# Kernel optimization log

Hardware: AMD Instinct MI355X
Metric: run time of the kernel (lower is better)

Reference implementation:

```python
import jax, jax.numpy as jnp
import numpy as np

D_VISION = 1024
D_BRANCH = 256
N_BRANCHES = 4
N_HEADS = 4
HEAD_DIM = D_BRANCH // N_HEADS
DIVERSITY_WEIGHT = 0.1
LN_EPS = 1e-5


def setup_inputs() -> dict:
    key = jax.random.key(0)
    ks = jax.random.split(key, 8)
    B, T, N = 8, 16, 256
    frame_patches = jax.random.normal(ks[0], (B, T, N, D_VISION), dtype=jnp.float32)
    # LayerNorm params (shared input_norm)
    ln_gamma = jnp.ones((D_VISION,), jnp.float32)
    ln_beta = jnp.zeros((D_VISION,), jnp.float32)
    # Per-branch params stacked on a leading branch dim
    query = jax.random.normal(ks[1], (N_BRANCHES, N_HEADS, HEAD_DIM), jnp.float32) * 0.02
    wstd = 1.0 / np.sqrt(D_VISION)
    Wk = jax.random.uniform(ks[2], (N_BRANCHES, D_VISION, D_BRANCH), jnp.float32, -wstd, wstd)
    bk = jax.random.uniform(ks[3], (N_BRANCHES, D_BRANCH), jnp.float32, -wstd, wstd)
    Wv = jax.random.uniform(ks[4], (N_BRANCHES, D_VISION, D_BRANCH), jnp.float32, -wstd, wstd)
    bv = jax.random.uniform(ks[5], (N_BRANCHES, D_BRANCH), jnp.float32, -wstd, wstd)
    ostd = 1.0 / np.sqrt(D_BRANCH)
    Wo = jax.random.uniform(ks[6], (N_BRANCHES, D_BRANCH, D_BRANCH), jnp.float32, -ostd, ostd)
    bo = jax.random.uniform(ks[7], (N_BRANCHES, D_BRANCH), jnp.float32, -ostd, ostd)
    return dict(frame_patches=frame_patches, ln_gamma=ln_gamma, ln_beta=ln_beta,
                query=query, Wk=Wk, bk=bk, Wv=Wv, bv=bv, Wo=Wo, bo=bo)


def _layernorm(x, g, b):
    mu = jnp.mean(x, axis=-1, keepdims=True)
    var = jnp.var(x, axis=-1, keepdims=True)
    return (x - mu) * jax.lax.rsqrt(var + LN_EPS) * g + b


def reference(frame_patches, ln_gamma, ln_beta, query, Wk, bk, Wv, bv, Wo, bo):
    B, T, N, D = frame_patches.shape
    nb, H, hd = query.shape
    db = H * hd
    scale = hd ** -0.5
    x = _layernorm(frame_patches.reshape(B * T, N, D), ln_gamma, ln_beta)  # (BT, N, D)
    # Batched k/v projections across all branches (the fusion opportunity)
    k = (jnp.einsum('bpd,ndk->nbpk', x, Wk) + bk[:, None, None, :]).reshape(nb, B * T, N, H, hd)
    v = (jnp.einsum('bpd,ndk->nbpk', x, Wv) + bv[:, None, None, :]).reshape(nb, B * T, N, H, hd)
    # Single learnable query per (branch, head) attends over patches
    scores = jnp.einsum('nbphd,nhd->nbhp', k, query) * scale  # (nb, BT, H, N)
    attn = jax.nn.softmax(scores, axis=-1)
    attn_avg = attn.mean(axis=2)  # (nb, BT, N) head-averaged, pre-dropout
    # Dropout is inference no-op (eval mode)
    pooled = jnp.einsum('nbhp,nbphd->nbhd', attn, v).reshape(nb, B * T, db)
    out = jnp.einsum('nbk,nkj->nbj', pooled, Wo) + bo[:, None, :]  # (nb, BT, db)
    streams = out.transpose(1, 0, 2).reshape(B, T, nb, db)
    # Diversity loss: mean pairwise cosine similarity of attention distributions
    norms = jnp.maximum(jnp.linalg.norm(attn_avg, axis=-1, keepdims=True), 1e-8)
    a = attn_avg / norms
    sims = jnp.einsum('ibn,jbn->ijb', a, a).mean(axis=-1)  # (nb, nb)
    mask = jnp.triu(jnp.ones((nb, nb), attn_avg.dtype), k=1)
    diversity_loss = DIVERSITY_WEIGHT * (sims * mask).sum() / mask.sum()
    return streams, diversity_loss
```

## Files before the change

### kernel.cpp

```cpp
#include <hip/hip_runtime.h>
#include <stdint.h>

#define BT      128
#define NPATCH  256
#define DV      1024
#define NB      4
#define DB      256
#define NH16    16
#define SCALE   0.125f
#define LNEPS   1e-5f

#define OFF_BWS    16384u
#define OFF_PSC    24608u
#define OFF_DRAW   25120u
#define OFF_STATS  549408u
#define OFF_W      614944u
#define OFF_CV     1139232u
#define OFF_DIV    1141280u
#define OFF_XBAR   1142048u
#define OFF_POOL   9530656u
#define XSLICE     2097152u

#define LROW 264

typedef short bf16x8 __attribute__((ext_vector_type(8)));
typedef float f32x4  __attribute__((ext_vector_type(4)));

__device__ __forceinline__ short f2bf(float f) {
    union { float f; unsigned u; } v; v.f = f;
    unsigned u = v.u;
    unsigned r = (u + 0x7fffu + ((u >> 16) & 1u)) >> 16;
    return (short)r;
}

__device__ __forceinline__ unsigned pk2(float lo, float hi) {
    union { float f; unsigned u; } a, b; a.f = lo; b.f = hi;
    return __builtin_amdgcn_perm(b.u, a.u, 0x07060302u);
}

__global__ __launch_bounds__(256) void kP(const float* __restrict__ Wk,
                                          const float* __restrict__ q,
                                          const float* __restrict__ g,
                                          const float* __restrict__ b,
                                          float* __restrict__ ws) {
    const int nh = blockIdx.x >> 4, ich = blockIdx.x & 15;
    const int n = nh >> 2, h = nh & 3;
    __shared__ float qs[64];
    __shared__ float redS[4], redC[4];
    const int t = threadIdx.x;
    if (t < 64) qs[t] = q[nh * 64 + t];
    __syncthreads();
    const int r = t >> 2, qd = t & 3;
    const int i = ich * 64 + r;
    const float* wrow = Wk + ((size_t)n * DV + i) * DB + h * 64 + qd * 16;
    float acc = 0.f;
    #pragma unroll
    for (int d = 0; d < 16; d += 4) {
        float4 w4 = *(const float4*)(wrow + d);
        acc += w4.x * qs[qd * 16 + d]     + w4.y * qs[qd * 16 + d + 1]
             + w4.z * qs[qd * 16 + d + 2] + w4.w * qs[qd * 16 + d + 3];
    }
    acc += __shfl_xor(acc, 1);
    acc += __shfl_xor(acc, 2);
    float gw = g[i] * acc;
    if (qd == 0) {
        unsigned short* bws = (unsigned short*)(ws + OFF_BWS);
        const int kt = i >> 5, oct = (r >> 3) & 3, j = r & 7;
        bws[((kt * 64 + oct * 16 + nh) << 3) + j] = (unsigned short)f2bf(gw);
    }
    float mS = (qd == 0) ? gw : 0.f;
    float mC = (qd == 0) ? b[i] * acc : 0.f;
    #pragma unroll
    for (int dd = 4; dd < 64; dd <<= 1) { mS += __shfl_xor(mS, dd); mC += __shfl_xor(mC, dd); }
    const int wave = t >> 6, lane = t & 63;
    if (lane == 0) { redS[wave] = mS; redC[wave] = mC; }
    __syncthreads();
    if (t == 0) {
        ws[OFF_PSC + (nh * 16 + ich) * 2 + 0] = redS[0] + redS[1] + redS[2] + redS[3];
        ws[OFF_PSC + (nh * 16 + ich) * 2 + 1] = redC[0] + redC[1] + redC[2] + redC[3];
    }
}

__global__ __launch_bounds__(256) void kA(const float* __restrict__ x,
                                          float* __restrict__ ws) {
    __shared__ unsigned short xs[64 * LROW];
    const int t = threadIdx.x;
    const int wv = t >> 6, lane = t & 63;
    const int m = lane & 15, oct = lane >> 4;
    const int row0 = blockIdx.x * 64;
    const bf16x8* bfp = (const bf16x8*)((const unsigned short*)(ws + OFF_BWS));
    const float* xb = x + (size_t)row0 * DV;

    float sum[16], sq[16];
    #pragma unroll
    for (int i = 0; i < 16; ++i) { sum[i] = 0.f; sq[i] = 0.f; }
    f32x4 acc = {0.f, 0.f, 0.f, 0.f};
    float4 r[16];

    auto loadr = [&](int c) {
        #pragma unroll
        for (int i = 0; i < 16; ++i)
            r[i] = *(const float4*)(xb + (size_t)(i * 4 + wv) * DV + c * 256 + lane * 4);
    };
    auto commit = [&]() {
        #pragma unroll
        for (int i = 0; i < 16; ++i) {
            float4 v = r[i];
            sum[i] += v.x + v.y + v.z + v.w;
            sq[i]  += v.x * v.x + v.y * v.y + v.z * v.z + v.w * v.w;
            uint2 pk; pk.x = pk2(v.x, v.y); pk.y = pk2(v.z, v.w);
            *(uint2*)&xs[(i * 4 + wv) * LROW + lane * 4] = pk;
        }
    };
    auto comp = [&](int c) {
        #pragma unroll
        for (int kt = 0; kt < 8; ++kt) {
            bf16x8 af = *(const bf16x8*)&xs[(wv * 16 + m) * LROW + kt * 32 + oct * 8];
            bf16x8 bf = bfp[(c * 8 + kt) * 64 + lane];
            acc = __builtin_amdgcn_mfma_f32_16x16x32_bf16(af, bf, acc, 0, 0, 0);
        }
    };

    loadr(0);
    for (int c = 0; c < 4; ++c) {
        __syncthreads();
        commit();
        __syncthreads();
        if (c < 3) loadr(c + 1);
        comp(c);
    }

    #pragma unroll
    for (int r2 = 0; r2 < 4; ++r2)
        ws[OFF_DRAW + (size_t)(row0 + wv * 16 + oct * 4 + r2) * 16 + m] = acc[r2];

    #pragma unroll
    for (int i = 0; i < 16; ++i) {
        float s = sum[i], q2 = sq[i];
        #pragma unroll
        for (int d = 1; d < 64; d <<= 1) { s += __shfl_xor(s, d); q2 += __shfl_xor(q2, d); }
        if (lane == 0) {
            const int row = row0 + i * 4 + wv;
            const float mu  = s * (1.f / 1024.f);
            const float var = q2 * (1.f / 1024.f) - mu * mu;
            float2 st; st.x = mu; st.y = rsqrtf(var + LNEPS);
            *(float2*)(ws + OFF_STATS + (size_t)row * 2) = st;
        }
    }
}

__global__ __launch_bounds__(256) void kC(const float* __restrict__ x,
                                          const float* __restrict__ q,
                                          const float* __restrict__ bk,
                                          float* __restrict__ ws) {
    const int bt = blockIdx.x;
    const int qq = blockIdx.y;
    const int t = threadIdx.x;
    __shared__ __attribute__((aligned(16))) float s_s[NH16 * NPATCH];
    __shared__ __attribute__((aligned(16))) float aavg[NB * NPATCH];
    __shared__ __attribute__((aligned(16))) float w_s[64 * 16];
    __shared__ __attribute__((aligned(16))) float rstd_s[NPATCH];
    __shared__ __attribute__((aligned(16))) float mrs[NPATCH];
    __shared__ float Ss[NH16], Cbs[NH16];

    {
        const int nh = t >> 4, ich = t & 15;
        float S = ws[OFF_PSC + t * 2 + 0];
        float C = ws[OFF_PSC + t * 2 + 1];
        const int n2 = nh >> 2, h2 = nh & 3;
        const float* bkp = bk + n2 * DB + h2 * 64 + ich * 4;
        const float* qp  = q + nh * 64 + ich * 4;
        C += bkp[0] * qp[0] + bkp[1] * qp[1] + bkp[2] * qp[2] + bkp[3] * qp[3];
        #pragma unroll
        for (int d = 1; d < 16; d <<= 1) { S += __shfl_xor(S, d); C += __shfl_xor(C, d); }
        if (ich == 0) { Ss[nh] = S; Cbs[nh] = C; }
    }
    const size_t row = (size_t)bt * NPATCH + t;
    const float2 st = *(const float2*)(ws + OFF_STATS + row * 2);
    rstd_s[t] = st.y;
    mrs[t] = st.x * st.y;
    __syncthreads();

    const float* dr = ws + OFF_DRAW + row * 16;
    #pragma unroll
    for (int nh = 0; nh < NH16; ++nh)
        s_s[nh * NPATCH + t] = (st.y * (dr[nh] - st.x * Ss[nh]) + Cbs[nh]) * SCALE;
    __syncthreads();

    const int wave = t >> 6, lane = t & 63;
    for (int r = 0; r < 4; ++r) {
        const int nh = wave * 4 + r;
        float4 v = *(float4*)&s_s[nh * NPATCH + lane * 4];
        float mx = fmaxf(fmaxf(v.x, v.y), fmaxf(v.z, v.w));
        for (int d = 1; d < 64; d <<= 1) mx = fmaxf(mx, __shfl_xor(mx, d));
        float e0 = __expf(v.x - mx), e1 = __expf(v.y - mx);
        float e2 = __expf(v.z - mx), e3 = __expf(v.w - mx);
        float s = e0 + e1 + e2 + e3;
        for (int d = 1; d < 64; d <<= 1) s += __shfl_xor(s, d);
        float inv = 1.f / s;
        float4 a; a.x = e0 * inv; a.y = e1 * inv; a.z = e2 * inv; a.w = e3 * inv;
        *(float4*)&s_s[nh * NPATCH + lane * 4] = a;
    }
    __syncthreads();

    if (qq == 0) {
        for (int r = 0; r < 4; ++r) {
            const int nh = wave * 4 + r;
            float4 a4 = *(float4*)&s_s[nh * NPATCH + lane * 4];
            float4 m4 = *(float4*)&mrs[lane * 4];
            float dd = a4.x * m4.x + a4.y * m4.y + a4.z * m4.z + a4.w * m4.w;
            for (int d = 1; d < 64; d <<= 1) dd += __shfl_xor(dd, d);
            if (lane == 0) ws[OFF_CV + bt * NH16 + nh] = dd;
        }
        #pragma unroll
        for (int nb2 = 0; nb2 < NB; ++nb2)
            aavg[nb2 * NPATCH + t] = 0.25f * (s_s[(nb2 * 4 + 0) * NPATCH + t] + s_s[(nb2 * 4 + 1) * NPATCH + t]
                                            + s_s[(nb2 * 4 + 2) * NPATCH + t] + s_s[(nb2 * 4 + 3) * NPATCH + t]);
        __syncthreads();
        if (wave == 0) {
            float nrm[NB];
            #pragma unroll
            for (int nb2 = 0; nb2 < NB; ++nb2) {
                float4 v = *(float4*)&aavg[nb2 * NPATCH + lane * 4];
                float ss = v.x * v.x + v.y * v.y + v.z * v.z + v.w * v.w;
                for (int d = 1; d < 64; d <<= 1) ss += __shfl_xor(ss, d);
                nrm[nb2] = fmaxf(sqrtf(ss), 1e-8f);
            }
            int pi = 0;
            for (int i2 = 0; i2 < NB; ++i2)
                for (int j2 = i2 + 1; j2 < NB; ++j2) {
                    float4 va = *(float4*)&aavg[i2 * NPATCH + lane * 4];
                    float4 vb = *(float4*)&aavg[j2 * NPATCH + lane * 4];
                    float dd = va.x * vb.x + va.y * vb.y + va.z * vb.z + va.w * vb.w;
                    for (int d = 1; d < 64; d <<= 1) dd += __shfl_xor(dd, d);
                    if (lane == 0) ws[OFF_DIV + bt * 6 + pi] = dd / (nrm[i2] * nrm[j2]);
                    ++pi;
                }
        }
    }

    for (int idx = t; idx < 1024; idx += 256) {
        const int p = idx >> 4, nh = idx & 15;
        w_s[idx] = s_s[nh * NPATCH + qq * 64 + p] * rstd_s[qq * 64 + p];
    }
    __syncthreads();

    float4 acc[16];
    #pragma unroll
    for (int i = 0; i < 16; ++i) { acc[i].x = 0.f; acc[i].y = 0.f; acc[i].z = 0.f; acc[i].w = 0.f; }
    const float* xp = x + (size_t)(bt * NPATCH + qq * 64) * DV + t * 4;
    #define FMA4(k, wgt, xv) acc[k].x += (wgt) * xv.x; acc[k].y += (wgt) * xv.y; \
                             acc[k].z += (wgt) * xv.z; acc[k].w += (wgt) * xv.w;
    #define PBLOCK(p, xv) { \
        float4 a0 = *(const float4*)&w_s[(p) * 16 + 0]; \
        float4 a1 = *(const float4*)&w_s[(p) * 16 + 4]; \
        float4 a2 = *(const float4*)&w_s[(p) * 16 + 8]; \
        float4 a3 = *(const float4*)&w_s[(p) * 16 + 12]; \
        FMA4(0, a0.x, xv)  FMA4(1, a0.y, xv)  FMA4(2, a0.z, xv)  FMA4(3, a0.w, xv) \
        FMA4(4, a1.x, xv)  FMA4(5, a1.y, xv)  FMA4(6, a1.z, xv)  FMA4(7, a1.w, xv) \
        FMA4(8, a2.x, xv)  FMA4(9, a2.y, xv)  FMA4(10, a2.z, xv) FMA4(11, a2.w, xv) \
        FMA4(12, a3.x, xv) FMA4(13, a3.y, xv) FMA4(14, a3.z, xv) FMA4(15, a3.w, xv) }
    for (int p = 0; p < 16; ++p) {
        float4 xv0 = *(const float4*)(xp + (size_t)(p +  0) * DV);
        float4 xv1 = *(const float4*)(xp + (size_t)(p + 16) * DV);
        float4 xv2 = *(const float4*)(xp + (size_t)(p + 32) * DV);
        float4 xv3 = *(const float4*)(xp + (size_t)(p + 48) * DV);
        PBLOCK(p, xv0)
        PBLOCK(p + 16, xv1)
        PBLOCK(p + 32, xv2)
        PBLOCK(p + 48, xv3)
    }
    #undef PBLOCK
    #undef FMA4
    #pragma unroll
    for (int nh = 0; nh < 16; ++nh)
        *(float4*)(ws + OFF_XBAR + (size_t)qq * XSLICE
                   + ((size_t)bt * NH16 + nh) * DV + t * 4) = acc[nh];
}

__global__ __launch_bounds__(256) void kD1(const float* __restrict__ Wv,
                                           const float* __restrict__ g,
                                           const float* __restrict__ b,
                                           const float* __restrict__ bv,
                                           float* __restrict__ ws) {
    const int nh = blockIdx.x & 15, btg = blockIdx.x >> 4;
    const int n = nh >> 2, h = nh & 3;
    const int bt0 = btg * 4, cb = h * 64;
    __shared__ __attribute__((aligned(16))) float xs[4][1024];
    __shared__ __attribute__((aligned(16))) float gs[1024], bs[1024];
    __shared__ float red[4][64][6];
    const int t = threadIdx.x;
    for (int e = t; e < 1024; e += 256) {
        const int bt = e >> 8, i4 = e & 255;
        const size_t b0 = OFF_XBAR + ((size_t)(bt0 + bt) * NH16 + nh) * DV + i4 * 4;
        float4 s = {0.f, 0.f, 0.f, 0.f};
        #pragma unroll
        for (int qq = 0; qq < 4; ++qq) {
            float4 v = *(const float4*)(ws + b0 + (size_t)qq * XSLICE);
            s.x += v.x; s.y += v.y; s.z += v.z; s.w += v.w;
        }
        *(float4*)&xs[bt][i4 * 4] = s;
    }
    for (int e = t; e < 1024; e += 256) { gs[e] = g[e]; bs[e] = b[e]; }
    __syncthreads();
    const int c = t & 63, sub = t >> 6;
    float acc[4];
    #pragma unroll
    for (int l = 0; l < 4; ++l) acc[l] = 0.f;
    float gv = 0.f, bvv = 0.f;
    const float* wvp = Wv + ((size_t)n * DV + sub * 256) * DB + cb + c;
    const int ib0 = sub * 256;
    #pragma unroll 2
    for (int gidx = 0; gidx < 64; ++gidx) {
        const int ib = ib0 + gidx * 4;
        float w0 = wvp[(size_t)(gidx * 4 + 0) * DB];
        float w1 = wvp[(size_t)(gidx * 4 + 1) * DB];
        float w2 = wvp[(size_t)(gidx * 4 + 2) * DB];
        float w3 = wvp[(size_t)(gidx * 4 + 3) * DB];
        float4 g4 = *(const float4*)&gs[ib];
        float4 b4 = *(const float4*)&bs[ib];
        float q0 = g4.x * w0, q1 = g4.y * w1, q2 = g4.z * w2, q3 = g4.w * w3;
        gv  += q0 + q1 + q2 + q3;
        bvv += b4.x * w0 + b4.y * w1 + b4.z * w2 + b4.w * w3;
        #pragma unroll
        for (int l = 0; l < 4; ++l) {
            float4 xr = *(const float4*)&xs[l][ib];
            acc[l] += xr.x * q0 + xr.y * q1 + xr.z * q2 + xr.w * q3;
        }
    }
    #pragma unroll
    for (int l = 0; l < 4; ++l) red[sub][c][l] = acc[l];
    red[sub][c][4] = gv; red[sub][c][5] = bvv;
    __syncthreads();
    const int c2 = t & 63, l = t >> 6;
    float gvS = red[0][c2][4] + red[1][c2][4] + red[2][c2][4] + red[3][c2][4];
    float bvS = red[0][c2][5] + red[1][c2][5] + red[2][c2][5] + red[3][c2][5];
    float base = bv[n * DB + cb + c2] + bvS;
    float p = red[0][c2][l] + red[1][c2][l] + red[2][c2][l] + red[3][c2][l];
    float C = ws[OFF_CV + (bt0 + l) * NH16 + nh];
    ws[OFF_POOL + ((size_t)n * BT + bt0 + l) * DB + cb + c2] = p - C * gvS + base;
}

__global__ __launch_bounds__(256) void kD2(const float* __restrict__ Wo,
                                           const float* __restrict__ bo,
                                           const float* __restrict__ ws,
                                           float* __restrict__ out) {
    const int btg = blockIdx.x & 15, jq = (blockIdx.x >> 4) & 3, n = blockIdx.x >> 6;
    const int bt0 = btg * 8, j0 = jq * 64;
    __shared__ __attribute__((aligned(16))) float ps[8][256];
    __shared__ float red[4][64][8];
    __shared__ float dred[4];
    const int t = threadIdx.x;
    for (int e = t; e < 512; e += 256) {
        const int bt = e >> 6, c4 = e & 63;
        *(float4*)&ps[bt][c4 * 4] =
            *(const float4*)(ws + OFF_POOL + ((size_t)n * BT + bt0 + bt) * DB + c4 * 4);
    }
    float dacc = 0.f;
    if (blockIdx.x == 0)
        for (int idx = t; idx < 768; idx += 256) dacc += ws[OFF_DIV + idx];
    for (int d = 1; d < 64; d <<= 1) dacc += __shfl_xor(dacc, d);
    if ((t & 63) == 0) dred[t >> 6] = dacc;
    __syncthreads();
    if (blockIdx.x == 0 && t == 0)
        out[131072] = 0.1f * (dred[0] + dred[1] + dred[2] + dred[3]) / 768.f;
    const int j = t & 63, sub = t >> 6;
    float acc[8];
    #pragma unroll
    for (int l = 0; l < 8; ++l) acc[l] = 0.f;
    const float* wop = Wo + ((size_t)n * DB + sub * 64) * DB + j0 + j;
    const int cb0 = sub * 64;
    #pragma unroll 2
    for (int gidx = 0; gidx < 16; ++gidx) {
        const int cb = cb0 + gidx * 4;
        float w0 = wop[(size_t)(gidx * 4 + 0) * DB];
        float w1 = wop[(size_t)(gidx * 4 + 1) * DB];
        float w2 = wop[(size_t)(gidx * 4 + 2) * DB];
        float w3 = wop[(size_t)(gidx * 4 + 3) * DB];
        #pragma unroll
        for (int l = 0; l < 8; ++l) {
            float4 pr = *(const float4*)&ps[l][cb];
            acc[l] += pr.x * w0 + pr.y * w1 + pr.z * w2 + pr.w * w3;
        }
    }
    #pragma unroll
    for (int l = 0; l < 8; ++l) red[sub][j][l] = acc[l];
    __syncthreads();
    const int j2 = t & 63, l0 = t >> 6;
    float bov = bo[n * DB + j0 + j2];
    #pragma unroll
    for (int li = 0; li < 2; ++li) {
        const int l = l0 + li * 4;
        float o = red[0][j2][l] + red[1][j2][l] + red[2][j2][l] + red[3][j2][l] + bov;
        out[((size_t)(bt0 + l) * NB + n) * DB + j0 + j2] = o;
    }
}

extern "C" void kernel_launch(void* const* d_in, const int* in_sizes, int n_in,
                              void* d_out, int out_size, void* d_ws, size_t ws_size,
                              hipStream_t stream) {
    const float* x  = (const float*)d_in[0];
    const float* g  = (const float*)d_in[1];
    const float* b  = (const float*)d_in[2];
    const float* q  = (const float*)d_in[3];
    const float* Wk = (const float*)d_in[4];
    const float* bk = (const float*)d_in[5];
    const float* Wv = (const float*)d_in[6];
    const float* bv = (const float*)d_in[7];
    const float* Wo = (const float*)d_in[8];
    const float* bo = (const float*)d_in[9];
    float* out = (float*)d_out;
    float* ws  = (float*)d_ws;

    hipLaunchKernelGGL(kP,  dim3(256),    dim3(256), 0, stream, Wk, q, g, b, ws);
    hipLaunchKernelGGL(kA,  dim3(512),    dim3(256), 0, stream, x, ws);
    hipLaunchKernelGGL(kC,  dim3(128, 4), dim3(256), 0, stream, x, q, bk, ws);
    hipLaunchKernelGGL(kD1, dim3(512),    dim3(256), 0, stream, Wv, g, b, bv, ws);
    hipLaunchKernelGGL(kD2, dim3(256),    dim3(256), 0, stream, Wo, bo, ws, out);
}
```

Baseline: 281.0 us.

## Fuse five kernels into one persistent kernel with grid-wide barriers

Merges the five separate launches (Wk·q projection, x·B MFMA with LN stats, softmax/xbar accumulation, Wv pooling, Wo output) into a single 512-block kernel that separates phases with atomic-counter grid barriers. A memset resets the barrier counters before each launch. The intent is to remove launch gaps and tail effects between the stages. The risk is that the spin barriers deadlock or serialize if all 512 blocks are not co-resident; launch_bounds(256,2) and the spin cap only mitigate this.

Result: slower. 554.6 us (+97.4%).

```diff
diff --git a/kernel.cpp b/kernel.cpp
--- a/kernel.cpp
+++ b/kernel.cpp
@@ -9,12 +9,12 @@
 #define NH16    16
 #define SCALE   0.125f
 #define LNEPS   1e-5f
+#define NBLK    512
 
 #define OFF_BWS    16384u
 #define OFF_PSC    24608u
 #define OFF_DRAW   25120u
 #define OFF_STATS  549408u
-#define OFF_W      614944u
 #define OFF_CV     1139232u
 #define OFF_DIV    1141280u
 #define OFF_XBAR   1142048u
@@ -38,361 +38,384 @@
     return __builtin_amdgcn_perm(b.u, a.u, 0x07060302u);
 }
 
-__global__ __launch_bounds__(256) void kP(const float* __restrict__ Wk,
-                                          const float* __restrict__ q,
-                                          const float* __restrict__ g,
-                                          const float* __restrict__ b,
-                                          float* __restrict__ ws) {
-    const int nh = blockIdx.x >> 4, ich = blockIdx.x & 15;
-    const int n = nh >> 2, h = nh & 3;
-    __shared__ float qs[64];
-    __shared__ float redS[4], redC[4];
-    const int t = threadIdx.x;
-    if (t < 64) qs[t] = q[nh * 64 + t];
+__device__ __forceinline__ void gridbar(int* bar, int phase) {
     __syncthreads();
-    const int r = t >> 2, qd = t & 3;
-    const int i = ich * 64 + r;
-    const float* wrow = Wk + ((size_t)n * DV + i) * DB + h * 64 + qd * 16;
-    float acc = 0.f;
-    #pragma unroll
-    for (int d = 0; d < 16; d += 4) {
-        float4 w4 = *(const float4*)(wrow + d);
-        acc += w4.x * qs[qd * 16 + d]     + w4.y * qs[qd * 16 + d + 1]
-             + w4.z * qs[qd * 16 + d + 2] + w4.w * qs[qd * 16 + d + 3];
-    }
-    acc += __shfl_xor(acc, 1);
-    acc += __shfl_xor(acc, 2);
-    float gw = g[i] * acc;
-    if (qd == 0) {
-        unsigned short* bws = (unsigned short*)(ws + OFF_BWS);
-        const int kt = i >> 5, oct = (r >> 3) & 3, j = r & 7;
-        bws[((kt * 64 + oct * 16 + nh) << 3) + j] = (unsigned short)f2bf(gw);
-    }
-    float mS = (qd == 0) ? gw : 0.f;
-    float mC = (qd == 0) ? b[i] * acc : 0.f;
-    #pragma unroll
-    for (int dd = 4; dd < 64; dd <<= 1) { mS += __shfl_xor(mS, dd); mC += __shfl_xor(mC, dd); }
-    const int wave = t >> 6, lane = t & 63;
-    if (lane == 0) { redS[wave] = mS; redC[wave] = mC; }
+    if (threadIdx.x == 0) {
+        __threadfence();
+        __hip_atomic_fetch_add(&bar[phase], 1, __ATOMIC_ACQ_REL,
+                               __HIP_MEMORY_SCOPE_AGENT);
+        int spins = 0;
+        while (__hip_atomic_load(&bar[phase], __ATOMIC_ACQUIRE,
+                                 __HIP_MEMORY_SCOPE_AGENT) < NBLK
+               && spins < (1 << 21)) {
+            ++spins;
+            __builtin_amdgcn_s_sleep(8);
+        }
+        __threadfence();
+    }
     __syncthreads();
-    if (t == 0) {
-        ws[OFF_PSC + (nh * 16 + ich) * 2 + 0] = redS[0] + redS[1] + redS[2] + redS[3];
-        ws[OFF_PSC + (nh * 16 + ich) * 2 + 1] = redC[0] + redC[1] + redC[2] + redC[3];
-    }
 }
 
-__global__ __launch_bounds__(256) void kA(const float* __restrict__ x,
-                                          float* __restrict__ ws) {
-    __shared__ unsigned short xs[64 * LROW];
-    const int t = threadIdx.x;
-    const int wv = t >> 6, lane = t & 63;
-    const int m = lane & 15, oct = lane >> 4;
-    const int row0 = blockIdx.x * 64;
-    const bf16x8* bfp = (const bf16x8*)((const unsigned short*)(ws + OFF_BWS));
-    const float* xb = x + (size_t)row0 * DV;
-
-    float sum[16], sq[16];
-    #pragma unroll
-    for (int i = 0; i < 16; ++i) { sum[i] = 0.f; sq[i] = 0.f; }
-    f32x4 acc = {0.f, 0.f, 0.f, 0.f};
-    float4 r[16];
-
-    auto loadr = [&](int c) {
-        #pragma unroll
-        for (int i = 0; i < 16; ++i)
-            r[i] = *(const float4*)(xb + (size_t)(i * 4 + wv) * DV + c * 256 + lane * 4);
-    };
-    auto commit = [&]() {
+__global__ __launch_bounds__(256, 2) void kMega(
+    const float* __restrict__ x,  const float* __restrict__ g,
+    const float* __restrict__ b,  const float* __restrict__ q,
+    const float* __restrict__ Wk, const float* __restrict__ bk,
+    const float* __restrict__ Wv, const float* __restrict__ bv,
+    const float* __restrict__ Wo, const float* __restrict__ bo,
+    float* __restrict__ ws, float* __restrict__ out)
+{
+    __shared__ __attribute__((aligned(16))) float smf[8448];
+    int* bar = (int*)ws;
+    const int t   = threadIdx.x;
+    const int blk = blockIdx.x;
+
+    if (blk < 256) {
+        float* qs   = smf;
+        float* redS = smf + 64;
+        float* redC = smf + 68;
+        const int nh = blk >> 4, ich = blk & 15;
+        const int n = nh >> 2, h = nh & 3;
+        if (t < 64) qs[t] = q[nh * 64 + t];
+        __syncthreads();
+        const int r = t >> 2, qd = t & 3;
+        const int i = ich * 64 + r;
+        const float* wrow = Wk + ((size_t)n * DV + i) * DB + h * 64 + qd * 16;
+        float acc = 0.f;
+        #pragma unroll
+        for (int d = 0; d < 16; d += 4) {
+            float4 w4 = *(const float4*)(wrow + d);
+            acc += w4.x * qs[qd * 16 + d]     + w4.y * qs[qd * 16 + d + 1]
+                 + w4.z * qs[qd * 16 + d + 2] + w4.w * qs[qd * 16 + d + 3];
+        }
+        acc += __shfl_xor(acc, 1);
+        acc += __shfl_xor(acc, 2);
+        float gw = g[i] * acc;
+        if (qd == 0) {
+            unsigned short* bws = (unsigned short*)(ws + OFF_BWS);
+            const int kt = i >> 5, oct = (r >> 3) & 3, j = r & 7;
+            bws[((kt * 64 + oct * 16 + nh) << 3) + j] = (unsigned short)f2bf(gw);
+        }
+        float mS = (qd == 0) ? gw : 0.f;
+        float mC = (qd == 0) ? b[i] * acc : 0.f;
+        #pragma unroll
+        for (int dd = 4; dd < 64; dd <<= 1) { mS += __shfl_xor(mS, dd); mC += __shfl_xor(mC, dd); }
+        const int wave = t >> 6, lane = t & 63;
+        if (lane == 0) { redS[wave] = mS; redC[wave] = mC; }
+        __syncthreads();
+        if (t == 0) {
+            ws[OFF_PSC + (nh * 16 + ich) * 2 + 0] = redS[0] + redS[1] + redS[2] + redS[3];
+            ws[OFF_PSC + (nh * 16 + ich) * 2 + 1] = redC[0] + redC[1] + redC[2] + redC[3];
+        }
+    }
+    gridbar(bar, 0);
+
+    {
+        unsigned short* xs = (unsigned short*)smf;
+        const int wv = t >> 6, lane = t & 63;
+        const int m = lane & 15, oct = lane >> 4;
+        const int row0 = blk * 64;
+        const bf16x8* bfp = (const bf16x8*)((const unsigned short*)(ws + OFF_BWS));
+        const float* xb = x + (size_t)row0 * DV;
+
+        float sum[16], sq[16];
+        #pragma unroll
+        for (int i = 0; i < 16; ++i) { sum[i] = 0.f; sq[i] = 0.f; }
+        f32x4 acc = {0.f, 0.f, 0.f, 0.f};
+        float4 r[16];
+
+        auto loadr = [&](int c) {
+            #pragma unroll
+            for (int i = 0; i < 16; ++i)
+                r[i] = *(const float4*)(xb + (size_t)(i * 4 + wv) * DV + c * 256 + lane * 4);
+        };
+        auto commit = [&]() {
+            #pragma unroll
+            for (int i = 0; i < 16; ++i) {
+                float4 v = r[i];
+                sum[i] += v.x + v.y + v.z + v.w;
+                sq[i]  += v.x * v.x + v.y * v.y + v.z * v.z + v.w * v.w;
+                uint2 pk; pk.x = pk2(v.x, v.y); pk.y = pk2(v.z, v.w);
+                *(uint2*)&xs[(i * 4 + wv) * LROW + lane * 4] = pk;
+            }
+        };
+        auto comp = [&](int c) {
+            #pragma unroll
+            for (int kt = 0; kt < 8; ++kt) {
+                bf16x8 af = *(const bf16x8*)&xs[(wv * 16 + m) * LROW + kt * 32 + oct * 8];
+                bf16x8 bf = bfp[(c * 8 + kt) * 64 + lane];
+                acc = __builtin_amdgcn_mfma_f32_16x16x32_bf16(af, bf, acc, 0, 0, 0);
+            }
+        };
+
+        loadr(0);
+        for (int c = 0; c < 4; ++c) {
+            __syncthreads();
+            commit();
+            __syncthreads();
+            if (c < 3) loadr(c + 1);
+            comp(c);
+        }
+
+        #pragma unroll
+        for (int r2 = 0; r2 < 4; ++r2)
+            ws[OFF_DRAW + (size_t)(row0 + wv * 16 + oct * 4 + r2) * 16 + m] = acc[r2];
+
         #pragma unroll
         for (int i = 0; i < 16; ++i) {
-            float4 v = r[i];
-            sum[i] += v.x + v.y + v.z + v.w;
-            sq[i]  += v.x * v.x + v.y * v.y + v.z * v.z + v.w * v.w;
-            uint2 pk; pk.x = pk2(v.x, v.y); pk.y = pk2(v.z, v.w);
-            *(uint2*)&xs[(i * 4 + wv) * LROW + lane * 4] = pk;
-        }
-    };
-    auto comp = [&](int c) {
-        #pragma unroll
-        for (int kt = 0; kt < 8; ++kt) {
-            bf16x8 af = *(const bf16x8*)&xs[(wv * 16 + m) * LROW + kt * 32 + oct * 8];
-            bf16x8 bf = bfp[(c * 8 + kt) * 64 + lane];
-            acc = __builtin_amdgcn_mfma_f32_16x16x32_bf16(af, bf, acc, 0, 0, 0);
-        }
-    };
-
-    loadr(0);
-    for (int c = 0; c < 4; ++c) {
-        __syncthreads();
-        commit();
-        __syncthreads();
-        if (c < 3) loadr(c + 1);
-        comp(c);
-    }
-
-    #pragma unroll
-    for (int r2 = 0; r2 < 4; ++r2)
-        ws[OFF_DRAW + (size_t)(row0 + wv * 16 + oct * 4 + r2) * 16 + m] = acc[r2];
-
-    #pragma unroll
-    for (int i = 0; i < 16; ++i) {
-        float s = sum[i], q2 = sq[i];
-        #pragma unroll
-        for (int d = 1; d < 64; d <<= 1) { s += __shfl_xor(s, d); q2 += __shfl_xor(q2, d); }
-        if (lane == 0) {
-            const int row = row0 + i * 4 + wv;
-            const float mu  = s * (1.f / 1024.f);
-            const float var = q2 * (1.f / 1024.f) - mu * mu;
-            float2 st; st.x = mu; st.y = rsqrtf(var + LNEPS);
-            *(float2*)(ws + OFF_STATS + (size_t)row * 2) = st;
-        }
-    }
-}
-
-__global__ __launch_bounds__(256) void kC(const float* __restrict__ x,
-                                          const float* __restrict__ q,
-                                          const float* __restrict__ bk,
-                                          float* __restrict__ ws) {
-    const int bt = blockIdx.x;
-    const int qq = blockIdx.y;
-    const int t = threadIdx.x;
-    __shared__ __attribute__((aligned(16))) float s_s[NH16 * NPATCH];
-    __shared__ __attribute__((aligned(16))) float aavg[NB * NPATCH];
-    __shared__ __attribute__((aligned(16))) float w_s[64 * 16];
-    __shared__ __attribute__((aligned(16))) float rstd_s[NPATCH];
-    __shared__ __attribute__((aligned(16))) float mrs[NPATCH];
-    __shared__ float Ss[NH16], Cbs[NH16];
+            float s = sum[i], q2 = sq[i];
+            #pragma unroll
+            for (int d = 1; d < 64; d <<= 1) { s += __shfl_xor(s, d); q2 += __shfl_xor(q2, d); }
+            if (lane == 0) {
+                const int row = row0 + i * 4 + wv;
+                const float mu  = s * (1.f / 1024.f);
+                const float var = q2 * (1.f / 1024.f) - mu * mu;
+                float2 st; st.x = mu; st.y = rsqrtf(var + LNEPS);
+                *(float2*)(ws + OFF_STATS + (size_t)row * 2) = st;
+            }
+        }
+    }
+    gridbar(bar, 1);
 
     {
-        const int nh = t >> 4, ich = t & 15;
-        float S = ws[OFF_PSC + t * 2 + 0];
-        float C = ws[OFF_PSC + t * 2 + 1];
-        const int n2 = nh >> 2, h2 = nh & 3;
-        const float* bkp = bk + n2 * DB + h2 * 64 + ich * 4;
-        const float* qp  = q + nh * 64 + ich * 4;
-        C += bkp[0] * qp[0] + bkp[1] * qp[1] + bkp[2] * qp[2] + bkp[3] * qp[3];
-        #pragma unroll
-        for (int d = 1; d < 16; d <<= 1) { S += __shfl_xor(S, d); C += __shfl_xor(C, d); }
-        if (ich == 0) { Ss[nh] = S; Cbs[nh] = C; }
-    }
-    const size_t row = (size_t)bt * NPATCH + t;
-    const float2 st = *(const float2*)(ws + OFF_STATS + row * 2);
-    rstd_s[t] = st.y;
-    mrs[t] = st.x * st.y;
-    __syncthreads();
-
-    const float* dr = ws + OFF_DRAW + row * 16;
-    #pragma unroll
-    for (int nh = 0; nh < NH16; ++nh)
-        s_s[nh * NPATCH + t] = (st.y * (dr[nh] - st.x * Ss[nh]) + Cbs[nh]) * SCALE;
-    __syncthreads();
-
-    const int wave = t >> 6, lane = t & 63;
-    for (int r = 0; r < 4; ++r) {
-        const int nh = wave * 4 + r;
-        float4 v = *(float4*)&s_s[nh * NPATCH + lane * 4];
-        float mx = fmaxf(fmaxf(v.x, v.y), fmaxf(v.z, v.w));
-        for (int d = 1; d < 64; d <<= 1) mx = fmaxf(mx, __shfl_xor(mx, d));
-        float e0 = __expf(v.x - mx), e1 = __expf(v.y - mx);
-        float e2 = __expf(v.z - mx), e3 = __expf(v.w - mx);
-        float s = e0 + e1 + e2 + e3;
-        for (int d = 1; d < 64; d <<= 1) s += __shfl_xor(s, d);
-        float inv = 1.f / s;
-        float4 a; a.x = e0 * inv; a.y = e1 * inv; a.z = e2 * inv; a.w = e3 * inv;
-        *(float4*)&s_s[nh * NPATCH + lane * 4] = a;
-    }
-    __syncthreads();
-
-    if (qq == 0) {
+        const int bt = blk & 127;
+        const int qq = blk >> 7;
+        float* s_s    = smf;
+        float* aavg   = smf + 4096;
+        float* w_s    = smf + 5120;
+        float* rstd_s = smf + 6144;
+        float* mrs    = smf + 6400;
+        float* Ss     = smf + 6656;
+        float* Cbs    = smf + 6672;
+
+        {
+            const int nh = t >> 4, ich = t & 15;
+            float S = ws[OFF_PSC + t * 2 + 0];
+            float C = ws[OFF_PSC + t * 2 + 1];
+            const int n2 = nh >> 2, h2 = nh & 3;
+            const float* bkp = bk + n2 * DB + h2 * 64 + ich * 4;
+            const float* qp  = q + nh * 64 + ich * 4;
+            C += bkp[0] * qp[0] + bkp[1] * qp[1] + bkp[2] * qp[2] + bkp[3] * qp[3];
+            #pragma unroll
+            for (int d = 1; d < 16; d <<= 1) { S += __shfl_xor(S, d); C += __shfl_xor(C, d); }
+            if (ich == 0) { Ss[nh] = S; Cbs[nh] = C; }
+        }
+        const size_t row = (size_t)bt * NPATCH + t;
+        const float2 st = *(const float2*)(ws + OFF_STATS + row * 2);
+        rstd_s[t] = st.y;
+        mrs[t] = st.x * st.y;
+        __syncthreads();
+
+        const float* dr = ws + OFF_DRAW + row * 16;
+        #pragma unroll
+        for (int nh = 0; nh < NH16; ++nh)
+            s_s[nh * NPATCH + t] = (st.y * (dr[nh] - st.x * Ss[nh]) + Cbs[nh]) * SCALE;
+        __syncthreads();
+
+        const int wave = t >> 6, lane = t & 63;
         for (int r = 0; r < 4; ++r) {
             const int nh = wave * 4 + r;
-            float4 a4 = *(float4*)&s_s[nh * NPATCH + lane * 4];
-            float4 m4 = *(float4*)&mrs[lane * 4];
-            float dd = a4.x * m4.x + a4.y * m4.y + a4.z * m4.z + a4.w * m4.w;
-            for (int d = 1; d < 64; d <<= 1) dd += __shfl_xor(dd, d);
-            if (lane == 0) ws[OFF_CV + bt * NH16 + nh] = dd;
-        }
-        #pragma unroll
-        for (int nb2 = 0; nb2 < NB; ++nb2)
-            aavg[nb2 * NPATCH + t] = 0.25f * (s_s[(nb2 * 4 + 0) * NPATCH + t] + s_s[(nb2 * 4 + 1) * NPATCH + t]
-                                            + s_s[(nb2 * 4 + 2) * NPATCH + t] + s_s[(nb2 * 4 + 3) * NPATCH + t]);
-        __syncthreads();
-        if (wave == 0) {
-            float nrm[NB];
-            #pragma unroll
-            for (int nb2 = 0; nb2 < NB; ++nb2) {
-                float4 v = *(float4*)&aavg[nb2 * NPATCH + lane * 4];
-                float ss = v.x * v.x + v.y * v.y + v.z * v.z + v.w * v.w;
-                for (int d = 1; d < 64; d <<= 1) ss += __shfl_xor(ss, d);
-                nrm[nb2] = fmaxf(sqrtf(ss), 1e-8f);
-            }
-            int pi = 0;
-            for (int i2 = 0; i2 < NB; ++i2)
-                for (int j2 = i2 + 1; j2 < NB; ++j2) {
-                    float4 va = *(float4*)&aavg[i2 * NPATCH + lane * 4];
-                    float4 vb = *(float4*)&aavg[j2 * NPATCH + lane * 4];
-                    float dd = va.x * vb.x + va.y * vb.y + va.z * vb.z + va.w * vb.w;
-                    for (int d = 1; d < 64; d <<= 1) dd += __shfl_xor(dd, d);
-                    if (lane == 0) ws[OFF_DIV + bt * 6 + pi] = dd / (nrm[i2] * nrm[j2]);
-                    ++pi;
+            float4 v = *(float4*)&s_s[nh * NPATCH + lane * 4];
+            float mx = fmaxf(fmaxf(v.x, v.y), fmaxf(v.z, v.w));
+            for (int d = 1; d < 64; d <<= 1) mx = fmaxf(mx, __shfl_xor(mx, d));
+            float e0 = __expf(v.x - mx), e1 = __expf(v.y - mx);
+            float e2 = __expf(v.z - mx), e3 = __expf(v.w - mx);
+            float s = e0 + e1 + e2 + e3;
+            for (int d = 1; d < 64; d <<= 1) s += __shfl_xor(s, d);
+            float inv = 1.f / s;
+            float4 a; a.x = e0 * inv; a.y = e1 * inv; a.z = e2 * inv; a.w = e3 * inv;
+            *(float4*)&s_s[nh * NPATCH + lane * 4] = a;
+        }
+        __syncthreads();
+
+        if (qq == 0) {
+            for (int r = 0; r < 4; ++r) {
+                const int nh = wave * 4 + r;
+                float4 a4 = *(float4*)&s_s[nh * NPATCH + lane * 4];
+                float4 m4 = *(float4*)&mrs[lane * 4];
+                float dd = a4.x * m4.x + a4.y * m4.y + a4.z * m4.z + a4.w * m4.w;
+                for (int d = 1; d < 64; d <<= 1) dd += __shfl_xor(dd, d);
+                if (lane == 0) ws[OFF_CV + bt * NH16 + nh] = dd;
+            }
+            #pragma unroll
+            for (int nb2 = 0; nb2 < NB; ++nb2)
+                aavg[nb2 * NPATCH + t] = 0.25f * (s_s[(nb2 * 4 + 0) * NPATCH + t] + s_s[(nb2 * 4 + 1) * NPATCH + t]
+                                                + s_s[(nb2 * 4 + 2) * NPATCH + t] + s_s[(nb2 * 4 + 3) * NPATCH + t]);
+            __syncthreads();
+            if (wave == 0) {
+                float nrm[NB];
+                #pragma unroll
+                for (int nb2 = 0; nb2 < NB; ++nb2) {
+                    float4 v = *(float4*)&aavg[nb2 * NPATCH + lane * 4];
+                    float ss = v.x * v.x + v.y * v.y + v.z * v.z + v.w * v.w;
+                    for (int d = 1; d < 64; d <<= 1) ss += __shfl_xor(ss, d);
+                    nrm[nb2] = fmaxf(sqrtf(ss), 1e-8f);
                 }
-        }
-    }
-
-    for (int idx = t; idx < 1024; idx += 256) {
-        const int p = idx >> 4, nh = idx & 15;
-        w_s[idx] = s_s[nh * NPATCH + qq * 64 + p] * rstd_s[qq * 64 + p];
-    }
-    __syncthreads();
-
-    float4 acc[16];
-    #pragma unroll
-    for (int i = 0; i < 16; ++i) { acc[i].x = 0.f; acc[i].y = 0.f; acc[i].z = 0.f; acc[i].w = 0.f; }
-    const float* xp = x + (size_t)(bt * NPATCH + qq * 64) * DV + t * 4;
-    #define FMA4(k, wgt, xv) acc[k].x += (wgt) * xv.x; acc[k].y += (wgt) * xv.y; \
-                             acc[k].z += (wgt) * xv.z; acc[k].w += (wgt) * xv.w;
-    #define PBLOCK(p, xv) { \
-        float4 a0 = *(const float4*)&w_s[(p) * 16 + 0]; \
-        float4 a1 = *(const float4*)&w_s[(p) * 16 + 4]; \
-        float4 a2 = *(const float4*)&w_s[(p) * 16 + 8]; \
-        float4 a3 = *(const float4*)&w_s[(p) * 16 + 12]; \
-        FMA4(0, a0.x, xv)  FMA4(1, a0.y, xv)  FMA4(2, a0.z, xv)  FMA4(3, a0.w, xv) \
-        FMA4(4, a1.x, xv)  FMA4(5, a1.y, xv)  FMA4(6, a1.z, xv)  FMA4(7, a1.w, xv) \
-        FMA4(8, a2.x, xv)  FMA4(9, a2.y, xv)  FMA4(10, a2.z, xv) FMA4(11, a2.w, xv) \
-        FMA4(12, a3.x, xv) FMA4(13, a3.y, xv) FMA4(14, a3.z, xv) FMA4(15, a3.w, xv) }
-    for (int p = 0; p < 16; ++p) {
-        float4 xv0 = *(const float4*)(xp + (size_t)(p +  0) * DV);
-        float4 xv1 = *(const float4*)(xp + (size_t)(p + 16) * DV);
-        float4 xv2 = *(const float4*)(xp + (size_t)(p + 32) * DV);
-        float4 xv3 = *(const float4*)(xp + (size_t)(p + 48) * DV);
-        PBLOCK(p, xv0)
-        PBLOCK(p + 16, xv1)
-        PBLOCK(p + 32, xv2)
-        PBLOCK(p + 48, xv3)
-    }
-    #undef PBLOCK
-    #undef FMA4
-    #pragma unroll
-    for (int nh = 0; nh < 16; ++nh)
-        *(float4*)(ws + OFF_XBAR + (size_t)qq * XSLICE
-                   + ((size_t)bt * NH16 + nh) * DV + t * 4) = acc[nh];
-}
-
-__global__ __launch_bounds__(256) void kD1(const float* __restrict__ Wv,
-                                           const float* __restrict__ g,
-                                           const float* __restrict__ b,
-                                           const float* __restrict__ bv,
-                                           float* __restrict__ ws) {
-    const int nh = blockIdx.x & 15, btg = blockIdx.x >> 4;
-    const int n = nh >> 2, h = nh & 3;
-    const int bt0 = btg * 4, cb = h * 64;
-    __shared__ __attribute__((aligned(16))) float xs[4][1024];
-    __shared__ __attribute__((aligned(16))) float gs[1024], bs[1024];
-    __shared__ float red[4][64][6];
-    const int t = threadIdx.x;
-    for (int e = t; e < 1024; e += 256) {
-        const int bt = e >> 8, i4 = e & 255;
-        const size_t b0 = OFF_XBAR + ((size_t)(bt0 + bt) * NH16 + nh) * DV + i4 * 4;
-        float4 s = {0.f, 0.f, 0.f, 0.f};
-        #pragma unroll
-        for (int qq = 0; qq < 4; ++qq) {
-            float4 v = *(const float4*)(ws + b0 + (size_t)qq * XSLICE);
-            s.x += v.x; s.y += v.y; s.z += v.z; s.w += v.w;
-        }
-        *(float4*)&xs[bt][i4 * 4] = s;
-    }
-    for (int e = t; e < 1024; e += 256) { gs[e] = g[e]; bs[e] = b[e]; }
-    __syncthreads();
-    const int c = t & 63, sub = t >> 6;
-    float acc[4];
-    #pragma unroll
-    for (int l = 0; l < 4; ++l) acc[l] = 0.f;
-    float gv = 0.f, bvv = 0.f;
-    const float* wvp = Wv + ((size_t)n * DV + sub * 256) * DB + cb + c;
-    const int ib0 = sub * 256;
-    #pragma unroll 2
-    for (int gidx = 0; gidx < 64; ++gidx) {
-        const int ib = ib0 + gidx * 4;
-        float w0 = wvp[(size_t)(gidx * 4 + 0) * DB];
-        float w1 = wvp[(size_t)(gidx * 4 + 1) * DB];
-        float w2 = wvp[(size_t)(gidx * 4 + 2) * DB];
-        float w3 = wvp[(size_t)(gidx * 4 + 3) * DB];
-        float4 g4 = *(const float4*)&gs[ib];
-        float4 b4 = *(const float4*)&bs[ib];
-        float q0 = g4.x * w0, q1 = g4.y * w1, q2 = g4.z * w2, q3 = g4.w * w3;
-        gv  += q0 + q1 + q2 + q3;
-        bvv += b4.x * w0 + b4.y * w1 + b4.z * w2 + b4.w * w3;
-        #pragma unroll
-        for (int l = 0; l < 4; ++l) {
-            float4 xr = *(const float4*)&xs[l][ib];
-            acc[l] += xr.x * q0 + xr.y * q1 + xr.z * q2 + xr.w * q3;
-        }
-    }
-    #pragma unroll
-    for (int l = 0; l < 4; ++l) red[sub][c][l] = acc[l];
-    red[sub][c][4] = gv; red[sub][c][5] = bvv;
-    __syncthreads();
-    const int c2 = t & 63, l = t >> 6;
-    float gvS = red[0][c2][4] + red[1][c2][4] + red[2][c2][4] + red[3][c2][4];
-    float bvS = red[0][c2][5] + red[1][c2][5] + red[2][c2][5] + red[3][c2][5];
-    float base = bv[n * DB + cb + c2] + bvS;
-    float p = red[0][c2][l] + red[1][c2][l] + red[2][c2][l] + red[3][c2][l];
-    float C = ws[OFF_CV + (bt0 + l) * NH16 + nh];
-    ws[OFF_POOL + ((size_t)n * BT + bt0 + l) * DB + cb + c2] = p - C * gvS + base;
-}
-
-__global__ __launch_bounds__(256) void kD2(const float* __restrict__ Wo,
-                                           const float* __restrict__ bo,
-                                           const float* __restrict__ ws,
-                                           float* __restrict__ out) {
-    const int btg = blockIdx.x & 15, jq = (blockIdx.x >> 4) & 3, n = blockIdx.x >> 6;
-    const int bt0 = btg * 8, j0 = jq * 64;
-    __shared__ __attribute__((aligned(16))) float ps[8][256];
-    __shared__ float red[4][64][8];
-    __shared__ float dred[4];
-    const int t = threadIdx.x;
-    for (int e = t; e < 512; e += 256) {
-        const int bt = e >> 6, c4 = e & 63;
-        *(float4*)&ps[bt][c4 * 4] =
-            *(const float4*)(ws + OFF_POOL + ((size_t)n * BT + bt0 + bt) * DB + c4 * 4);
-    }
-    float dacc = 0.f;
-    if (blockIdx.x == 0)
-        for (int idx = t; idx < 768; idx += 256) dacc += ws[OFF_DIV + idx];
-    for (int d = 1; d < 64; d <<= 1) dacc += __shfl_xor(dacc, d);
-    if ((t & 63) == 0) dred[t >> 6] = dacc;
-    __syncthreads();
-    if (blockIdx.x == 0 && t == 0)
-        out[131072] = 0.1f * (dred[0] + dred[1] + dred[2] + dred[3]) / 768.f;
-    const int j = t & 63, sub = t >> 6;
-    float acc[8];
-    #pragma unroll
-    for (int l = 0; l < 8; ++l) acc[l] = 0.f;
-    const float* wop = Wo + ((size_t)n * DB + sub * 64) * DB + j0 + j;
-    const int cb0 = sub * 64;
-    #pragma unroll 2
-    for (int gidx = 0; gidx < 16; ++gidx) {
-        const int cb = cb0 + gidx * 4;
-        float w0 = wop[(size_t)(gidx * 4 + 0) * DB];
-        float w1 = wop[(size_t)(gidx * 4 + 1) * DB];
-        float w2 = wop[(size_t)(gidx * 4 + 2) * DB];
-        float w3 = wop[(size_t)(gidx * 4 + 3) * DB];
-        #pragma unroll
-        for (int l = 0; l < 8; ++l) {
-            float4 pr = *(const float4*)&ps[l][cb];
-            acc[l] += pr.x * w0 + pr.y * w1 + pr.z * w2 + pr.w * w3;
-        }
-    }
-    #pragma unroll
-    for (int l = 0; l < 8; ++l) red[sub][j][l] = acc[l];
-    __syncthreads();
-    const int j2 = t & 63, l0 = t >> 6;
-    float bov = bo[n * DB + j0 + j2];
-    #pragma unroll
-    for (int li = 0; li < 2; ++li) {
-        const int l = l0 + li * 4;
-        float o = red[0][j2][l] + red[1][j2][l] + red[2][j2][l] + red[3][j2][l] + bov;
-        out[((size_t)(bt0 + l) * NB + n) * DB + j0 + j2] = o;
+                int pi = 0;
+                for (int i2 = 0; i2 < NB; ++i2)
+                    for (int j2 = i2 + 1; j2 < NB; ++j2) {
+                        float4 va = *(float4*)&aavg[i2 * NPATCH + lane * 4];
+                        float4 vb = *(float4*)&aavg[j2 * NPATCH + lane * 4];
+                        float dd = va.x * vb.x + va.y * vb.y + va.z * vb.z + va.w * vb.w;
+                        for (int d = 1; d < 64; d <<= 1) dd += __shfl_xor(dd, d);
+                        if (lane == 0) ws[OFF_DIV + bt * 6 + pi] = dd / (nrm[i2] * nrm[j2]);
+                        ++pi;
+                    }
+            }
+        }
+
+        for (int idx = t; idx < 1024; idx += 256) {
+            const int p = idx >> 4, nh = idx & 15;
+            w_s[idx] = s_s[nh * NPATCH + qq * 64 + p] * rstd_s[qq * 64 + p];
+        }
+        __syncthreads();
+
+        float4 acc[16];
+        #pragma unroll
+        for (int i = 0; i < 16; ++i) { acc[i].x = 0.f; acc[i].y = 0.f; acc[i].z = 0.f; acc[i].w = 0.f; }
+        const float* xp = x + (size_t)(bt * NPATCH + qq * 64) * DV + t * 4;
+        #define FMA4(k, wgt, xv) acc[k].x += (wgt) * xv.x; acc[k].y += (wgt) * xv.y; \
+                                 acc[k].z += (wgt) * xv.z; acc[k].w += (wgt) * xv.w;
+        #define PBLOCK(p, xv) { \
+            float4 a0 = *(const float4*)&w_s[(p) * 16 + 0]; \
+            float4 a1 = *(const float4*)&w_s[(p) * 16 + 4]; \
+            float4 a2 = *(const float4*)&w_s[(p) * 16 + 8]; \
+            float4 a3 = *(const float4*)&w_s[(p) * 16 + 12]; \
+            FMA4(0, a0.x, xv)  FMA4(1, a0.y, xv)  FMA4(2, a0.z, xv)  FMA4(3, a0.w, xv) \
+            FMA4(4, a1.x, xv)  FMA4(5, a1.y, xv)  FMA4(6, a1.z, xv)  FMA4(7, a1.w, xv) \
+            FMA4(8, a2.x, xv)  FMA4(9, a2.y, xv)  FMA4(10, a2.z, xv) FMA4(11, a2.w, xv) \
+            FMA4(12, a3.x, xv) FMA4(13, a3.y, xv) FMA4(14, a3.z, xv) FMA4(15, a3.w, xv) }
+        for (int p = 0; p < 16; ++p) {
+            float4 xv0 = *(const float4*)(xp + (size_t)(p +  0) * DV);
+            float4 xv1 = *(const float4*)(xp + (size_t)(p + 16) * DV);
+            float4 xv2 = *(const float4*)(xp + (size_t)(p + 32) * DV);
+            float4 xv3 = *(const float4*)(xp + (size_t)(p + 48) * DV);
+            PBLOCK(p, xv0)
+            PBLOCK(p + 16, xv1)
+            PBLOCK(p + 32, xv2)
+            PBLOCK(p + 48, xv3)
+        }
+        #undef PBLOCK
+        #undef FMA4
+        #pragma unroll
+        for (int nh = 0; nh < 16; ++nh)
+            *(float4*)(ws + OFF_XBAR + (size_t)qq * XSLICE
+                       + ((size_t)bt * NH16 + nh) * DV + t * 4) = acc[nh];
+    }
+    gridbar(bar, 2);
+
+    {
+        const int nh = blk & 15, btg = blk >> 4;
+        const int n = nh >> 2, h = nh & 3;
+        const int bt0 = btg * 4, cb = h * 64;
+        float* xs4 = smf;
+        float* gs  = smf + 4096;
+        float* bs  = smf + 5120;
+        float* red = smf + 6144;
+        #define RED1(s_, c_, l_) red[(((s_) * 64) + (c_)) * 6 + (l_)]
+        for (int e = t; e < 1024; e += 256) {
+            const int bt = e >> 8, i4 = e & 255;
+            const size_t b0 = OFF_XBAR + ((size_t)(bt0 + bt) * NH16 + nh) * DV + i4 * 4;
+            float4 s = {0.f, 0.f, 0.f, 0.f};
+            #pragma unroll
+            for (int qq = 0; qq < 4; ++qq) {
+                float4 v = *(const float4*)(ws + b0 + (size_t)qq * XSLICE);
+                s.x += v.x; s.y += v.y; s.z += v.z; s.w += v.w;
+            }
+            *(float4*)&xs4[bt * 1024 + i4 * 4] = s;
+        }
+        for (int e = t; e < 1024; e += 256) { gs[e] = g[e]; bs[e] = b[e]; }
+        __syncthreads();
+        const int c = t & 63, sub = t >> 6;
+        float acc[4];
+        #pragma unroll
+        for (int l = 0; l < 4; ++l) acc[l] = 0.f;
+        float gv = 0.f, bvv = 0.f;
+        const float* wvp = Wv + ((size_t)n * DV + sub * 256) * DB + cb + c;
+        const int ib0 = sub * 256;
+        #pragma unroll 2
+        for (int gidx = 0; gidx < 64; ++gidx) {
+            const int ib = ib0 + gidx * 4;
+            float w0 = wvp[(size_t)(gidx * 4 + 0) * DB];
+            float w1 = wvp[(size_t)(gidx * 4 + 1) * DB];
+            float w2 = wvp[(size_t)(gidx * 4 + 2) * DB];
+            float w3 = wvp[(size_t)(gidx * 4 + 3) * DB];
+            float4 g4 = *(const float4*)&gs[ib];
+            float4 b4 = *(const float4*)&bs[ib];
+            float q0 = g4.x * w0, q1 = g4.y * w1, q2 = g4.z * w2, q3 = g4.w * w3;
+            gv  += q0 + q1 + q2 + q3;
+            bvv += b4.x * w0 + b4.y * w1 + b4.z * w2 + b4.w * w3;
+            #pragma unroll
+            for (int l = 0; l < 4; ++l) {
+                const float* xr = &xs4[l * 1024 + ib];
+                acc[l] += xr[0] * q0 + xr[1] * q1 + xr[2] * q2 + xr[3] * q3;
+            }
+        }
+        #pragma unroll
+        for (int l = 0; l < 4; ++l) RED1(sub, c, l) = acc[l];
+        RED1(sub, c, 4) = gv; RED1(sub, c, 5) = bvv;
+        __syncthreads();
+        const int c2 = t & 63, l = t >> 6;
+        float gvS = RED1(0, c2, 4) + RED1(1, c2, 4) + RED1(2, c2, 4) + RED1(3, c2, 4);
+        float bvS = RED1(0, c2, 5) + RED1(1, c2, 5) + RED1(2, c2, 5) + RED1(3, c2, 5);
+        float base = bv[n * DB + cb + c2] + bvS;
+        float p = RED1(0, c2, l) + RED1(1, c2, l) + RED1(2, c2, l) + RED1(3, c2, l);
+        float C = ws[OFF_CV + (bt0 + l) * NH16 + nh];
+        ws[OFF_POOL + ((size_t)n * BT + bt0 + l) * DB + cb + c2] = p - C * gvS + base;
+        #undef RED1
+    }
+    gridbar(bar, 3);
+
+    if (blk < 256) {
+        const int btg = blk & 15, jq = (blk >> 4) & 3, n = blk >> 6;
+        const int bt0 = btg * 8, j0 = jq * 64;
+        float* ps   = smf;
+        float* red  = smf + 2048;
+        float* dred = smf + 4096;
+        #define RED2(s_, j_, l_) red[(((s_) * 64) + (j_)) * 8 + (l_)]
+        for (int e = t; e < 512; e += 256) {
+            const int bt = e >> 6, c4 = e & 63;
+            *(float4*)&ps[bt * 256 + c4 * 4] =
+                *(const float4*)(ws + OFF_POOL + ((size_t)n * BT + bt0 + bt) * DB + c4 * 4);
+        }
+        float dacc = 0.f;
+        if (blk == 0)
+            for (int idx = t; idx < 768; idx += 256) dacc += ws[OFF_DIV + idx];
+        for (int d = 1; d < 64; d <<= 1) dacc += __shfl_xor(dacc, d);
+        if ((t & 63) == 0) dred[t >> 6] = dacc;
+        __syncthreads();
+        if (blk == 0 && t == 0)
+            out[131072] = 0.1f * (dred[0] + dred[1] + dred[2] + dred[3]) / 768.f;
+        const int j = t & 63, sub = t >> 6;
+        float acc[8];
+        #pragma unroll
+        for (int l = 0; l < 8; ++l) acc[l] = 0.f;
+        const float* wop = Wo + ((size_t)n * DB + sub * 64) * DB + j0 + j;
+        const int cb0 = sub * 64;
+        #pragma unroll 2
+        for (int gidx = 0; gidx < 16; ++gidx) {
+            const int cb = cb0 + gidx * 4;
+            float w0 = wop[(size_t)(gidx * 4 + 0) * DB];
+            float w1 = wop[(size_t)(gidx * 4 + 1) * DB];
+            float w2 = wop[(size_t)(gidx * 4 + 2) * DB];
+            float w3 = wop[(size_t)(gidx * 4 + 3) * DB];
+            #pragma unroll
+            for (int l = 0; l < 8; ++l) {
+                const float* pr = &ps[l * 256 + cb];
+                acc[l] += pr[0] * w0 + pr[1] * w1 + pr[2] * w2 + pr[3] * w3;
+            }
+        }
+        #pragma unroll
+        for (int l = 0; l < 8; ++l) RED2(sub, j, l) = acc[l];
+        __syncthreads();
+        const int j2 = t & 63, l0 = t >> 6;
+        float bov = bo[n * DB + j0 + j2];
+        #pragma unroll
+        for (int li = 0; li < 2; ++li) {
+            const int l = l0 + li * 4;
+            float o = RED2(0, j2, l) + RED2(1, j2, l) + RED2(2, j2, l) + RED2(3, j2, l) + bov;
+            out[((size_t)(bt0 + l) * NB + n) * DB + j0 + j2] = o;
+        }
+        #undef RED2
     }
 }
 
@@ -412,9 +435,7 @@
     float* out = (float*)d_out;
     float* ws  = (float*)d_ws;
 
-    hipLaunchKernelGGL(kP,  dim3(256),    dim3(256), 0, stream, Wk, q, g, b, ws);
-    hipLaunchKernelGGL(kA,  dim3(512),    dim3(256), 0, stream, x, ws);
-    hipLaunchKernelGGL(kC,  dim3(128, 4), dim3(256), 0, stream, x, q, bk, ws);
-    hipLaunchKernelGGL(kD1, dim3(512),    dim3(256), 0, stream, Wv, g, b, bv, ws);
-    hipLaunchKernelGGL(kD2, dim3(256),    dim3(256), 0, stream, Wo, bo, ws, out);
+    hipMemsetAsync(d_ws, 0, 64, stream);
+    hipLaunchKernelGGL(kMega, dim3(NBLK), dim3(256), 0, stream,
+                       x, g, b, q, Wk, bk, Wv, bv, Wo, bo, ws, out);
 }
```
